# Kernel tuning notes

Measured on AMD Instinct MI355X. Metric: run time of the kernel, lower is better.

Reference implementation:

```python
import jax, jax.numpy as jnp
import numpy as np

B, S, T, D = 64, 256, 8, 256
E, M = 500000, 2048
NEG_INF = -10000000000.0


def setup_inputs() -> dict:
    key = jax.random.key(0)
    ks = jax.random.split(key, 9)
    token_reprs = jax.random.normal(ks[0], (B, S, T, D), dtype=jnp.float32)
    w1 = jax.random.normal(ks[1], (D, D // 2), dtype=jnp.float32) * (1.0 / np.sqrt(D))
    b1 = jnp.zeros((D // 2,), dtype=jnp.float32)
    w2 = jax.random.normal(ks[2], (D // 2, 1), dtype=jnp.float32) * (1.0 / np.sqrt(D // 2))
    b2 = jnp.zeros((1,), dtype=jnp.float32)
    edge_index = jax.random.randint(ks[3], (2, E), 0, B * S, dtype=jnp.int32)
    lm_indices = jax.random.randint(ks[4], (M,), 0, B * S * T, dtype=jnp.int32)
    batch_pointers = jax.random.randint(ks[5], (M,), 0, B, dtype=jnp.int32)
    tree_padding_mask = jax.random.randint(ks[6], (B, S), 0, 2, dtype=jnp.int32).astype(jnp.bool_)
    return {
        "token_reprs": token_reprs,
        "w1": w1, "b1": b1, "w2": w2, "b2": b2,
        "edge_index": edge_index,
        "lm_indices": lm_indices,
        "batch_pointers": batch_pointers,
        "tree_padding_mask": tree_padding_mask,
    }


def reference(token_reprs, w1, b1, w2, b2, edge_index, lm_indices, batch_pointers, tree_padding_mask):
    b, s, t, d = token_reprs.shape
    # type representation is the first token of each type tree
    type_reprs = token_reprs[:, :, 0]                  # [B, S, D]
    flat_types = type_reprs.reshape(b * s, d)          # [B*S, D]

    # predict_lemmas: gather scope/goal reprs, elementwise multiply, 2-layer MLP
    scope_ids, goal_ids = edge_index[0], edge_index[1]
    h = flat_types[scope_ids] * flat_types[goal_ids]   # [E, D]
    h = h @ w1 + b1                                    # [E, D//2] (Dropout is identity in eval)
    lemmas = (h @ w2 + b2)[:, 0]                       # [E]

    # predict_masks: gather masked token reprs + per-tree candidates, dot, mask
    mask_reprs = token_reprs.reshape(b * s * t, d)[lm_indices]  # [M, D]
    candidates = type_reprs[batch_pointers]            # [M, S, D]
    candidate_mask = tree_padding_mask[batch_pointers] # [M, S]
    lm_preds = jnp.einsum('md,msd->ms', mask_reprs, candidates)
    lm_preds = jnp.where(candidate_mask, lm_preds, NEG_INF)
    return lemmas, lm_preds
```

## Files before the change

kernel.cpp:

```cpp
#include <hip/hip_runtime.h>

#define DD 256
#define SS 256
#define BB 64
#define NEDGE 500000
#define MM 2048
#define NEG_INF -10000000000.0f
#define ROWF4 512
#define NROWS (BB * SS)

#define OFF_VC     0
#define OFF_MSORT  4096
#define OFF_BSTART (4096 + MM * 4)
#define OFF_ASLAB  (1 << 16)
#define OFF_P2     ((1 << 16) + (8 << 20))
#define OFF_MROWS  ((1 << 16) + (16 << 20))

__device__ __forceinline__ float bflo(unsigned u) { return __uint_as_float(u << 16); }
__device__ __forceinline__ float bfhi(unsigned u) { return __uint_as_float(u & 0xFFFF0000u); }
__device__ __forceinline__ unsigned short bf_rne(float f) {
    unsigned u = __float_as_uint(f);
    return (unsigned short)((u + 0x7FFFu + ((u >> 16) & 1u)) >> 16);
}
__device__ __forceinline__ unsigned pack2_rne(float a, float b) {
    return (unsigned)bf_rne(a) | ((unsigned)bf_rne(b) << 16);
}

__global__ void setup_k(const float* __restrict__ w1, const float* __restrict__ b1,
                        const float* __restrict__ w2, const float* __restrict__ b2,
                        const int* __restrict__ bp,
                        float* __restrict__ vc, int* __restrict__ msorted,
                        int* __restrict__ bstart) {
    const int t = threadIdx.x;
    if (blockIdx.x == 0) {
        float acc = 0.f;
        #pragma unroll 4
        for (int j = 0; j < DD / 2; ++j) acc += w1[t * (DD / 2) + j] * w2[j];
        vc[t] = acc;
        if (t == 0) {
            float c = b2[0];
            for (int j = 0; j < DD / 2; ++j) c += b1[j] * w2[j];
            vc[DD] = c;
        }
    } else {
        __shared__ int hist[BB];
        __shared__ int offs[BB + 1];
        if (t < BB) hist[t] = 0;
        __syncthreads();
        for (int m = t; m < MM; m += 256) atomicAdd(&hist[bp[m]], 1);
        __syncthreads();
        if (t == 0) {
            int acc = 0;
            for (int i = 0; i < BB; ++i) { offs[i] = acc; acc += hist[i]; }
            offs[BB] = acc;
        }
        __syncthreads();
        if (t < BB + 1) bstart[t] = offs[t];
        __syncthreads();
        for (int m = t; m < MM; m += 256) {
            int pos = atomicAdd(&offs[bp[m]], 1);
            msorted[pos] = m;
        }
    }
}

__global__ __launch_bounds__(256) void compact(
        const float* __restrict__ tok, const int* __restrict__ lmi,
        unsigned* __restrict__ aslab,
        unsigned* __restrict__ p2, unsigned* __restrict__ mrows) {
    const int lane = threadIdx.x & 63;
    const int w    = threadIdx.x >> 6;
    if (blockIdx.x < NROWS / 4) {
        const int row = blockIdx.x * 4 + w;
        const float4 a = ((const float4*)tok)[(size_t)row * ROWF4 + lane];
        unsigned p0 = pack2_rne(a.x, a.y), p1 = pack2_rne(a.z, a.w);
        const int k = lane >> 3, sub = lane & 7;
        const size_t si = (size_t)(k * NROWS + row) * 16 + sub * 2;
        aslab[si] = p0; aslab[si + 1] = p1;
        const size_t pi = (size_t)row * 128 + lane * 2;
        p2[pi] = p0; p2[pi + 1] = p1;
    } else {
        const int m = (blockIdx.x - NROWS / 4) * 4 + w;
        const float4 a = ((const float4*)(tok + (size_t)lmi[m] * DD))[lane];
        mrows[(size_t)m * 128 + lane * 2]     = pack2_rne(a.x, a.y);
        mrows[(size_t)m * 128 + lane * 2 + 1] = pack2_rne(a.z, a.w);
    }
}

__global__ __launch_bounds__(256) void edge_fused(
        const unsigned* __restrict__ aslab,
        const int* __restrict__ edges, const float* __restrict__ vc,
        float* __restrict__ out) {
    const int t = threadIdx.x;
    const int lane = t & 63, w = t >> 6;
    const int sub = lane & 7, j = lane >> 3;
    const int e0 = blockIdx.x * 256;
    __shared__ int sIdx[2][256];
    __shared__ float accs[256];
    const int e = e0 + t;
    const bool val = e < NEDGE;
    sIdx[0][t] = val ? __builtin_nontemporal_load(edges + e) : 0;
    sIdx[1][t] = val ? __builtin_nontemporal_load(edges + NEDGE + e) : 0;

    float4 v4[8];
    #pragma unroll
    for (int k = 0; k < 8; ++k) v4[k] = ((const float4*)vc)[k * 8 + sub];
    __syncthreads();

    float acc[8];
    #pragma unroll
    for (int i = 0; i < 8; ++i) acc[i] = 0.f;
    const int slotbase = w * 64 + j;

    #pragma unroll 1
    for (int k = 0; k < 8; ++k) {
        const unsigned* base = aslab + (size_t)k * NROWS * 16 + sub * 2;
        const float4 v = v4[k];
        #pragma unroll
        for (int i = 0; i < 8; ++i) {
            const int slot = slotbase + i * 8;
            const int sc = sIdx[0][slot];
            const int gl = sIdx[1][slot];
            const uint2 pu = *(const uint2*)(base + (size_t)sc * 16);
            const uint2 qu = *(const uint2*)(base + (size_t)gl * 16);
            acc[i] += (bflo(pu.x) * bflo(qu.x)) * v.x
                    + (bfhi(pu.x) * bfhi(qu.x)) * v.y
                    + (bflo(pu.y) * bflo(qu.y)) * v.z
                    + (bfhi(pu.y) * bfhi(qu.y)) * v.w;
        }
    }
    #pragma unroll
    for (int i = 0; i < 8; ++i) {
        float p = acc[i];
        p += __shfl_down(p, 4, 8);
        p += __shfl_down(p, 2, 8);
        p += __shfl_down(p, 1, 8);
        if (sub == 0) accs[slotbase + i * 8] = p;
    }
    __syncthreads();
    if (val) __builtin_nontemporal_store(accs[t] + vc[DD], out + e);
}

__global__ __launch_bounds__(256) void lm_gemm(
        const unsigned* __restrict__ p2,
        const unsigned* __restrict__ mrows,
        const int* __restrict__ msorted,
        const int* __restrict__ bstart,
        const int* __restrict__ tpm,
        float* __restrict__ out) {
    const int b  = blockIdx.x;
    const int st = blockIdx.y;
    const int ch = blockIdx.z;
    const int s0 = bstart[b], s1 = bstart[b + 1];
    const int base = s0 + ch * 32;
    if (base >= s1) return;
    const int nm = min(32, s1 - base);
    const int t = threadIdx.x;

    __shared__ unsigned lmaskU[32 * 132];
    __shared__ unsigned srowU[32 * 132];
    __shared__ int mids[32];
    __shared__ int sact[64];
    __shared__ int snact;

    if (t < 32) mids[t] = msorted[base + min(t, nm - 1)];
    if (t >= 64 && t < 128) {
        int lt = t - 64;
        bool act = tpm[b * SS + st * 64 + lt] != 0;
        unsigned long long mk = __ballot(act);
        if (act) sact[__popcll(mk & ((1ull << lt) - 1))] = lt;
        if (lt == 0) snact = (int)__popcll(mk);
    }
    __syncthreads();

    for (int f = t; f < nm * 32; f += 256) {
        int r = f >> 5, q = f & 31;
        *(uint4*)&lmaskU[r * 132 + q * 4] = ((const uint4*)mrows)[(size_t)mids[r] * 32 + q];
    }
    for (int f = t; f < nm * 64; f += 256) {
        int i = f >> 6, c = f & 63;
        if (!tpm[b * SS + st * 64 + c])
            out[(size_t)mids[i] * SS + st * 64 + c] = NEG_INF;
    }
    __syncthreads();

    const int nact = snact;
    const int i2 = t & 15, sg = t >> 4;

    for (int g = 0; g * 32 < nact; ++g) {
        if (g) __syncthreads();
        const int nv = min(32, nact - g * 32);
        for (int f = t; f < nv * 32; f += 256) {
            int r = f >> 5, q = f & 31;
            size_t row = (size_t)b * SS + st * 64 + sact[g * 32 + r];
            *(uint4*)&srowU[r * 132 + q * 4] = ((const uint4*)p2)[row * 32 + q];
        }
        __syncthreads();

        float a00 = 0.f, a01 = 0.f, a10 = 0.f, a11 = 0.f;
        #pragma unroll 4
        for (int stp = 0; stp < 32; ++stp) {
            const uint4 A0 = *(const uint4*)&lmaskU[i2 * 132 + stp * 4];
            const uint4 A1 = *(const uint4*)&lmaskU[(i2 + 16) * 132 + stp * 4];
            const uint4 B0 = *(const uint4*)&srowU[sg * 132 + stp * 4];
            const uint4 B1 = *(const uint4*)&srowU[(sg + 16) * 132 + stp * 4];
            float a0[8], a1[8], b0[8], b1[8];
            a0[0] = bflo(A0.x); a0[1] = bfhi(A0.x); a0[2] = bflo(A0.y); a0[3] = bfhi(A0.y);
            a0[4] = bflo(A0.z); a0[5] = bfhi(A0.z); a0[6] = bflo(A0.w); a0[7] = bfhi(A0.w);
            a1[0] = bflo(A1.x); a1[1] = bfhi(A1.x); a1[2] = bflo(A1.y); a1[3] = bfhi(A1.y);
            a1[4] = bflo(A1.z); a1[5] = bfhi(A1.z); a1[6] = bflo(A1.w); a1[7] = bfhi(A1.w);
            b0[0] = bflo(B0.x); b0[1] = bfhi(B0.x); b0[2] = bflo(B0.y); b0[3] = bfhi(B0.y);
            b0[4] = bflo(B0.z); b0[5] = bfhi(B0.z); b0[6] = bflo(B0.w); b0[7] = bfhi(B0.w);
            b1[0] = bflo(B1.x); b1[1] = bfhi(B1.x); b1[2] = bflo(B1.y); b1[3] = bfhi(B1.y);
            b1[4] = bflo(B1.z); b1[5] = bfhi(B1.z); b1[6] = bflo(B1.w); b1[7] = bfhi(B1.w);
            #pragma unroll
            for (int jj = 0; jj < 8; ++jj) {
                a00 = fmaf(a0[jj], b0[jj], a00);
                a01 = fmaf(a0[jj], b1[jj], a01);
                a10 = fmaf(a1[jj], b0[jj], a10);
                a11 = fmaf(a1[jj], b1[jj], a11);
            }
        }

        const int iA = g * 32 + sg, iB = iA + 16;
        if (i2 < nm) {
            size_t ob = (size_t)mids[i2] * SS + st * 64;
            if (iA < nact) out[ob + sact[iA]] = a00;
            if (iB < nact) out[ob + sact[iB]] = a01;
        }
        if (i2 + 16 < nm) {
            size_t ob = (size_t)mids[i2 + 16] * SS + st * 64;
            if (iA < nact) out[ob + sact[iA]] = a10;
            if (iB < nact) out[ob + sact[iB]] = a11;
        }
    }
}

extern "C" void kernel_launch(void* const* d_in, const int* in_sizes, int n_in,
                              void* d_out, int out_size, void* d_ws, size_t ws_size,
                              hipStream_t stream) {
    const float* tok = (const float*)d_in[0];
    const float* w1  = (const float*)d_in[1];
    const float* b1  = (const float*)d_in[2];
    const float* w2  = (const float*)d_in[3];
    const float* b2  = (const float*)d_in[4];
    const int* edges = (const int*)d_in[5];
    const int* lmi   = (const int*)d_in[6];
    const int* bp    = (const int*)d_in[7];
    const int* tpm   = (const int*)d_in[8];

    float* out_lemmas = (float*)d_out;
    float* out_lm     = (float*)d_out + NEDGE;

    char* ws = (char*)d_ws;
    float* vc        = (float*)(ws + OFF_VC);
    int* msorted     = (int*)(ws + OFF_MSORT);
    int* bstart      = (int*)(ws + OFF_BSTART);
    unsigned* aslab  = (unsigned*)(ws + OFF_ASLAB);
    unsigned* p2     = (unsigned*)(ws + OFF_P2);
    unsigned* mrows  = (unsigned*)(ws + OFF_MROWS);

    setup_k<<<2, 256, 0, stream>>>(w1, b1, w2, b2, bp, vc, msorted, bstart);
    compact<<<NROWS / 4 + MM / 4, 256, 0, stream>>>(tok, lmi, aslab, p2, mrows);
    edge_fused<<<(NEDGE + 255) / 256, 256, 0, stream>>>(aslab, edges, vc, out_lemmas);
    lm_gemm<<<dim3(BB, 4, 8), 256, 0, stream>>>(p2, mrows, msorted, bstart, tpm, out_lm);
}
```

Before: 279.4 us.

## Make edge kernel cooperative with grid syncs to walk bf16 slabs in lockstep

The edge kernel becomes a persistent cooperative launch: each block takes 512 edges, and the whole grid syncs after every two k-slabs. This keeps all blocks reading the same 2 MB slab window of the compacted bf16 table, so gathers should stay cache-resident. The setup kernel also replaces the per-thread serial w1·w2 dot products with wave-parallel shuffle reductions. In exchange there are three grid-wide barriers, more registers per thread (16 accumulators), and a hard dependence on the cooperative launch fitting all blocks resident at once.

```diff
diff --git a/kernel.cpp b/kernel.cpp
--- a/kernel.cpp
+++ b/kernel.cpp
@@ -1,4 +1,7 @@
 #include <hip/hip_runtime.h>
+#include <hip/hip_cooperative_groups.h>
+
+namespace cg = cooperative_groups;
 
 #define DD 256
 #define SS 256
@@ -9,6 +12,9 @@
 #define ROWF4 512
 #define NROWS (BB * SS)
 
+#define EPB 512
+#define NBLK ((NEDGE + EPB - 1) / EPB)
+
 #define OFF_VC     0
 #define OFF_MSORT  4096
 #define OFF_BSTART (4096 + MM * 4)
@@ -33,14 +39,30 @@
                         int* __restrict__ bstart) {
     const int t = threadIdx.x;
     if (blockIdx.x == 0) {
-        float acc = 0.f;
-        #pragma unroll 4
-        for (int j = 0; j < DD / 2; ++j) acc += w1[t * (DD / 2) + j] * w2[j];
-        vc[t] = acc;
-        if (t == 0) {
-            float c = b2[0];
-            for (int j = 0; j < DD / 2; ++j) c += b1[j] * w2[j];
-            vc[DD] = c;
+        __shared__ float sw2[DD / 2];
+        if (t < DD / 2) sw2[t] = w2[t];
+        __syncthreads();
+        const int lane = t & 63, w = t >> 6;
+        for (int r = w; r < DD; r += 4) {
+            float x = w1[r * (DD / 2) + lane] * sw2[lane]
+                    + w1[r * (DD / 2) + 64 + lane] * sw2[64 + lane];
+            x += __shfl_down(x, 32);
+            x += __shfl_down(x, 16);
+            x += __shfl_down(x, 8);
+            x += __shfl_down(x, 4);
+            x += __shfl_down(x, 2);
+            x += __shfl_down(x, 1);
+            if (lane == 0) vc[r] = x;
+        }
+        if (w == 0) {
+            float x = b1[lane] * sw2[lane] + b1[64 + lane] * sw2[64 + lane];
+            x += __shfl_down(x, 32);
+            x += __shfl_down(x, 16);
+            x += __shfl_down(x, 8);
+            x += __shfl_down(x, 4);
+            x += __shfl_down(x, 2);
+            x += __shfl_down(x, 1);
+            if (lane == 0) vc[DD] = x + b2[0];
         }
     } else {
         __shared__ int hist[BB];
@@ -87,38 +109,37 @@
     }
 }
 
-__global__ __launch_bounds__(256) void edge_fused(
+__global__ __launch_bounds__(256, 4) void edge_fused(
         const unsigned* __restrict__ aslab,
         const int* __restrict__ edges, const float* __restrict__ vc,
         float* __restrict__ out) {
+    cg::grid_group grid = cg::this_grid();
     const int t = threadIdx.x;
     const int lane = t & 63, w = t >> 6;
     const int sub = lane & 7, j = lane >> 3;
-    const int e0 = blockIdx.x * 256;
-    __shared__ int sIdx[2][256];
-    __shared__ float accs[256];
-    const int e = e0 + t;
-    const bool val = e < NEDGE;
-    sIdx[0][t] = val ? __builtin_nontemporal_load(edges + e) : 0;
-    sIdx[1][t] = val ? __builtin_nontemporal_load(edges + NEDGE + e) : 0;
-
-    float4 v4[8];
+    const int e0 = blockIdx.x * EPB;
+    __shared__ int sIdx[2][EPB];
+    __shared__ float accs[EPB];
+    for (int f = t; f < EPB; f += 256) {
+        const int e = e0 + f;
+        const bool val = e < NEDGE;
+        sIdx[0][f] = val ? __builtin_nontemporal_load(edges + e) : 0;
+        sIdx[1][f] = val ? __builtin_nontemporal_load(edges + NEDGE + e) : 0;
+    }
+    __syncthreads();
+
+    float acc[16];
     #pragma unroll
-    for (int k = 0; k < 8; ++k) v4[k] = ((const float4*)vc)[k * 8 + sub];
-    __syncthreads();
-
-    float acc[8];
-    #pragma unroll
-    for (int i = 0; i < 8; ++i) acc[i] = 0.f;
-    const int slotbase = w * 64 + j;
+    for (int i = 0; i < 16; ++i) acc[i] = 0.f;
+    const int slotbase = w * 8 + j;
 
     #pragma unroll 1
     for (int k = 0; k < 8; ++k) {
-        const unsigned* base = aslab + (size_t)k * NROWS * 16 + sub * 2;
-        const float4 v = v4[k];
+        const unsigned* base = aslab + (size_t)k * (NROWS * 16) + sub * 2;
+        const float4 v = ((const float4*)vc)[k * 8 + sub];
         #pragma unroll
-        for (int i = 0; i < 8; ++i) {
-            const int slot = slotbase + i * 8;
+        for (int i = 0; i < 16; ++i) {
+            const int slot = i * 32 + slotbase;
             const int sc = sIdx[0][slot];
             const int gl = sIdx[1][slot];
             const uint2 pu = *(const uint2*)(base + (size_t)sc * 16);
@@ -128,17 +149,23 @@
                     + (bflo(pu.y) * bflo(qu.y)) * v.z
                     + (bfhi(pu.y) * bfhi(qu.y)) * v.w;
         }
-    }
+        if ((k & 1) && k < 7) grid.sync();
+    }
+
     #pragma unroll
-    for (int i = 0; i < 8; ++i) {
+    for (int i = 0; i < 16; ++i) {
         float p = acc[i];
         p += __shfl_down(p, 4, 8);
         p += __shfl_down(p, 2, 8);
         p += __shfl_down(p, 1, 8);
-        if (sub == 0) accs[slotbase + i * 8] = p;
+        if (sub == 0) accs[i * 32 + slotbase] = p;
     }
     __syncthreads();
-    if (val) __builtin_nontemporal_store(accs[t] + vc[DD], out + e);
+    const float c = vc[DD];
+    for (int f = t; f < EPB; f += 256) {
+        const int e = e0 + f;
+        if (e < NEDGE) __builtin_nontemporal_store(accs[f] + c, out + e);
+    }
 }
 
 __global__ __launch_bounds__(256) void lm_gemm(
@@ -262,6 +289,16 @@
 
     setup_k<<<2, 256, 0, stream>>>(w1, b1, w2, b2, bp, vc, msorted, bstart);
     compact<<<NROWS / 4 + MM / 4, 256, 0, stream>>>(tok, lmi, aslab, p2, mrows);
-    edge_fused<<<(NEDGE + 255) / 256, 256, 0, stream>>>(aslab, edges, vc, out_lemmas);
+
+    {
+        const unsigned* a0 = aslab;
+        const int*      a1 = edges;
+        const float*    a2 = vc;
+        float*          a3 = out_lemmas;
+        void* args[4] = { (void*)&a0, (void*)&a1, (void*)&a2, (void*)&a3 };
+        hipLaunchCooperativeKernel((const void*)edge_fused, dim3(NBLK), dim3(256),
+                                   args, 0, stream);
+    }
+
     lm_gemm<<<dim3(BB, 4, 8), 256, 0, stream>>>(p2, mrows, msorted, bstart, tpm, out_lm);
 }
```

New measurement: 719.7 us. +157.6%, slower.
